# Kernel optimization log

Hardware: AMD Instinct MI355X
Metric: run time of the kernel (lower is better)

The kernel has to match this reference:

```python
import jax, jax.numpy as jnp
import numpy as np

N_NODES = 100000
N_EDGES = 1000000
D_IN = 64
D_OUT = 64


def setup_inputs() -> dict:
    key = jax.random.key(0)
    k_x, k_e, k_wl, k_bl, k_wr = jax.random.split(key, 5)
    x = jax.random.normal(k_x, (N_NODES, D_IN), dtype=jnp.float32)
    edge_index = jax.random.randint(k_e, (2, N_EDGES), 0, N_NODES, dtype=jnp.int64)
    scale = 1.0 / np.sqrt(D_IN)
    # SAGEConv params: lin_l (neighbor path, with bias), lin_r (root/self path, no bias)
    W_l = jax.random.uniform(k_wl, (D_OUT, D_IN), dtype=jnp.float32, minval=-scale, maxval=scale)
    b_l = jax.random.uniform(k_bl, (D_OUT,), dtype=jnp.float32, minval=-scale, maxval=scale)
    W_r = jax.random.uniform(k_wr, (D_OUT, D_IN), dtype=jnp.float32, minval=-scale, maxval=scale)
    return {"x": x, "edge_index": edge_index, "W_l": W_l, "b_l": b_l, "W_r": W_r}


def reference(x, edge_index, W_l, b_l, W_r):
    # PyG SAGEConv with mean aggregation:
    #   out = lin_l(mean_{j in N(i)} x_j) + lin_r(x_i);  then ReLU (from GCN.forward)
    src = edge_index[0]  # message sources
    dst = edge_index[1]  # aggregation targets
    n = x.shape[0]
    msg = x[src]  # [E, D_IN] gather
    agg = jax.ops.segment_sum(msg, dst, num_segments=n)  # [N, D_IN]
    deg = jax.ops.segment_sum(jnp.ones((src.shape[0],), x.dtype), dst, num_segments=n)
    mean = agg / jnp.maximum(deg, 1.0)[:, None]  # isolated nodes -> 0
    out = mean @ W_l.T + b_l + x @ W_r.T
    return jax.nn.relu(out)
```

## Files before the change

kernel.cpp:

```cpp
#include <hip/hip_runtime.h>

#define N_NODES 100000
#define N_EDGES 1000000
#define D 64

#define NFINE 782
#define CAP2 1536
#define CHUNK 4096
#define EDGE_BLOCKS 245
#define CONV_BLOCKS 6250
#define CONS_BLOCKS 782
#define STR 132

typedef unsigned short u16;
typedef unsigned int u32;
using bf16x8 = __attribute__((ext_vector_type(8))) short;
using f32x4  = __attribute__((ext_vector_type(4))) float;

__device__ __forceinline__ u16 f2bf(float f) {
    u32 u = __float_as_uint(f);
    return (u16)((u + 0x7FFF + ((u >> 16) & 1)) >> 16);
}
__device__ __forceinline__ float bf2f(u16 v) {
    return __uint_as_float(((u32)v) << 16);
}

__global__ __launch_bounds__(256) void conv_zero_kernel(
    const float* __restrict__ x, u16* __restrict__ xb,
    int* __restrict__ cur2) {
    if (blockIdx.x == CONV_BLOCKS) {
        for (int j = threadIdx.x; j < NFINE; j += 256) cur2[j] = 0;
        return;
    }
    int i = blockIdx.x * 256 + threadIdx.x;
    float4 v = ((const float4*)x)[i];
    ((ushort4*)xb)[i] = make_ushort4(f2bf(v.x), f2bf(v.y), f2bf(v.z), f2bf(v.w));
}

__global__ __launch_bounds__(1024) void build3_kernel(
    const int* __restrict__ ei, int* __restrict__ cur2,
    u32* __restrict__ pairs2) {
    __shared__ u32 sorted[CHUNK];
    __shared__ u16 binof[CHUNK];
    __shared__ int hist[NFINE];
    __shared__ int off_l[NFINE];
    __shared__ int cur_l[NFINE];
    __shared__ int base_g[NFINE];
    __shared__ int wsum[16];

    int b = blockIdx.x;
    int t = threadIdx.x;
    int ln = t & 63;
    int wv = t >> 6;

    const u32* uu = (const u32*)ei;
    int f = 1;
    #pragma unroll
    for (int i = 1; i < 16; i += 2)
        if (uu[i] != 0u) f = 0;

    if (t < NFINE) hist[t] = 0;
    __syncthreads();

    int e0 = b * CHUNK;
    int e1 = min(e0 + CHUNK, N_EDGES);
    int ne = e1 - e0;

    int srcv[4], dstv[4];
    #pragma unroll
    for (int i = 0; i < 4; i++) {
        int ee = e0 + t + i * 1024;
        bool ok = ee < e1;
        srcv[i] = ok ? (f ? ei[2 * ee] : ei[ee]) : 0;
        dstv[i] = ok ? (f ? ei[2 * (N_EDGES + ee)] : ei[N_EDGES + ee]) : -1;
    }
    #pragma unroll
    for (int i = 0; i < 4; i++)
        if (dstv[i] >= 0) atomicAdd(&hist[dstv[i] >> 7], 1);
    __syncthreads();

    int h = (t < NFINE) ? hist[t] : 0;
    int inc = h;
    #pragma unroll
    for (int o = 1; o < 64; o <<= 1) {
        int v = __shfl_up(inc, o);
        if (ln >= o) inc += v;
    }
    if (ln == 63) wsum[wv] = inc;
    __syncthreads();
    if (t < 16) {
        int w = wsum[t];
        int winc = w;
        #pragma unroll
        for (int o = 1; o < 16; o <<= 1) {
            int v = __shfl_up(winc, o);
            if (t >= o) winc += v;
        }
        wsum[t] = winc - w;
    }
    __syncthreads();
    if (t < NFINE) {
        int ex = inc - h + wsum[wv];
        off_l[t] = ex;
        cur_l[t] = ex;
        base_g[t] = h ? atomicAdd(&cur2[t], h) : 0;
    }
    __syncthreads();

    #pragma unroll
    for (int i = 0; i < 4; i++) {
        if (dstv[i] >= 0) {
            int fine = dstv[i] >> 7;
            int slot = atomicAdd(&cur_l[fine], 1);
            sorted[slot] = (u32)srcv[i] | ((u32)(dstv[i] & 127) << 17);
            binof[slot] = (u16)fine;
        }
    }
    __syncthreads();

    for (int i = t; i < ne; i += 1024) {
        int fine = binof[i];
        int pos = base_g[fine] + (i - off_l[fine]);
        if (pos < CAP2)
            pairs2[(size_t)fine * CAP2 + pos] = sorted[i];
    }
}

__global__ __launch_bounds__(1024, 8) void cons3_kernel(
    const u16* __restrict__ xb, const float* __restrict__ Wl,
    const float* __restrict__ bl, const float* __restrict__ Wr,
    const int* __restrict__ cur2, const u32* __restrict__ pairs2,
    float* __restrict__ out) {
    __shared__ u16 Bs[64 * STR];
    __shared__ u16 As[128 * STR];
    __shared__ int sorted_s[CAP2];
    __shared__ int deg_l[128];
    __shared__ int off_l[128];
    __shared__ int cur_l[128];

    int tid = threadIdx.x;
    int bin = blockIdx.x;
    int nbase = bin * 128;
    int lane = tid & 63;
    int wv = tid >> 6;

    if (tid < 128) { deg_l[tid] = 0; cur_l[tid] = 0; }
    for (int i = tid; i < CAP2; i += 1024) sorted_s[i] = 0;

    if (tid < 256) {
        int row = tid >> 2;
        int seg = tid & 3;
        const float4* wlf = (const float4*)Wl;
        const float4* wrf = (const float4*)Wr;
        #pragma unroll
        for (int j = 0; j < 4; j++) {
            float4 a = wlf[row * 16 + seg * 4 + j];
            float4 bq = wrf[row * 16 + seg * 4 + j];
            *(ushort4*)&Bs[row * STR + seg * 16 + j * 4] =
                make_ushort4(f2bf(a.x), f2bf(a.y), f2bf(a.z), f2bf(a.w));
            *(ushort4*)&Bs[row * STR + 64 + seg * 16 + j * 4] =
                make_ushort4(f2bf(bq.x), f2bf(bq.y), f2bf(bq.z), f2bf(bq.w));
        }
    }

    int cnt = min(cur2[bin], CAP2);
    const u32* pb = &pairs2[(size_t)bin * CAP2];
    u32 ve[2];
    #pragma unroll
    for (int i = 0; i < 2; i++) {
        int e = tid + i * 1024;
        ve[i] = (e < cnt) ? pb[e] : 0xFFFFFFFFu;
    }
    __syncthreads();

    #pragma unroll
    for (int i = 0; i < 2; i++)
        if (ve[i] != 0xFFFFFFFFu) atomicAdd(&deg_l[ve[i] >> 17], 1);
    __syncthreads();

    if (tid < 64) {
        int d0 = deg_l[2 * tid], d1 = deg_l[2 * tid + 1];
        int s = d0 + d1;
        int inc = s;
        #pragma unroll
        for (int o = 1; o < 64; o <<= 1) {
            int v = __shfl_up(inc, o);
            if (tid >= o) inc += v;
        }
        int ex = inc - s;
        off_l[2 * tid] = ex;
        off_l[2 * tid + 1] = ex + d0;
    }
    __syncthreads();

    #pragma unroll
    for (int i = 0; i < 2; i++) {
        u32 v = ve[i];
        if (v != 0xFFFFFFFFu) {
            int dl = (int)(v >> 17);
            int p = off_l[dl] + atomicAdd(&cur_l[dl], 1);
            sorted_s[p] = (int)(v & 0x1FFFFu);
        }
    }
    __syncthreads();

    int nl8 = lane >> 3;
    int c = lane & 7;
    int nl = wv * 8 + nl8;
    int n = nbase + nl;
    int d = deg_l[nl];
    int st = off_l[nl];

    int maxd = d;
    maxd = max(maxd, __shfl_xor(maxd, 8));
    maxd = max(maxd, __shfl_xor(maxd, 16));
    maxd = max(maxd, __shfl_xor(maxd, 32));

    float acc[8];
    #pragma unroll
    for (int j = 0; j < 8; j++) acc[j] = 0.0f;

    for (int k = 0; k < maxd; k += 2) {
        int i0 = max(st + min(k, d - 1), 0);
        int i1 = max(st + min(k + 1, d - 1), 0);
        int s0 = sorted_s[i0];
        int s1 = sorted_s[i1];
        float m0 = (k < d) ? 1.0f : 0.0f;
        float m1 = (k + 1 < d) ? 1.0f : 0.0f;
        bf16x8 r0 = *(const bf16x8*)&xb[(size_t)s0 * D + c * 8];
        bf16x8 r1 = *(const bf16x8*)&xb[(size_t)s1 * D + c * 8];
        #pragma unroll
        for (int j = 0; j < 8; j++)
            acc[j] = fmaf(m0, bf2f((u16)r0[j]), acc[j]);
        #pragma unroll
        for (int j = 0; j < 8; j++)
            acc[j] = fmaf(m1, bf2f((u16)r1[j]), acc[j]);
    }

    float inv = (d > 0) ? (1.0f / (float)d) : 0.0f;
    bf16x8 p;
    #pragma unroll
    for (int j = 0; j < 8; j++) p[j] = (short)f2bf(acc[j] * inv);
    *(bf16x8*)&As[nl * STR + c * 8] = p;
    bf16x8 xr = {0, 0, 0, 0, 0, 0, 0, 0};
    if (n < N_NODES) xr = *(const bf16x8*)&xb[(size_t)n * D + c * 8];
    *(bf16x8*)&As[nl * STR + 64 + c * 8] = xr;
    __syncthreads();

    int mtile = wv >> 1;
    int nt0 = (wv & 1) * 2;
    int lrow = lane & 15;
    int quad = lane >> 4;

    const u16* Ab  = &As[(mtile * 16 + lrow) * STR + quad * 8];
    const u16* Bb0 = &Bs[((nt0 + 0) * 16 + lrow) * STR + quad * 8];
    const u16* Bb1 = &Bs[((nt0 + 1) * 16 + lrow) * STR + quad * 8];

    float bias0 = bl[(nt0 + 0) * 16 + lrow];
    float bias1 = bl[(nt0 + 1) * 16 + lrow];
    f32x4 acc0 = {bias0, bias0, bias0, bias0};
    f32x4 acc1 = {bias1, bias1, bias1, bias1};

    #pragma unroll
    for (int kk = 0; kk < 4; kk++) {
        bf16x8 af = *(const bf16x8*)&Ab[kk * 32];
        bf16x8 b0 = *(const bf16x8*)&Bb0[kk * 32];
        bf16x8 b1 = *(const bf16x8*)&Bb1[kk * 32];
        acc0 = __builtin_amdgcn_mfma_f32_16x16x32_bf16(af, b0, acc0, 0, 0, 0);
        acc1 = __builtin_amdgcn_mfma_f32_16x16x32_bf16(af, b1, acc1, 0, 0, 0);
    }

    int node = nbase + mtile * 16 + quad * 4;
    #pragma unroll
    for (int r = 0; r < 4; r++) {
        if (node + r < N_NODES) {
            out[(size_t)(node + r) * D + (nt0 + 0) * 16 + lrow] = fmaxf(acc0[r], 0.0f);
            out[(size_t)(node + r) * D + (nt0 + 1) * 16 + lrow] = fmaxf(acc1[r], 0.0f);
        }
    }
}

extern "C" void kernel_launch(void* const* d_in, const int* in_sizes, int n_in,
                              void* d_out, int out_size, void* d_ws, size_t ws_size,
                              hipStream_t stream) {
    const float* x  = (const float*)d_in[0];
    const int*   ei = (const int*)d_in[1];
    const float* Wl = (const float*)d_in[2];
    const float* bl = (const float*)d_in[3];
    const float* Wr = (const float*)d_in[4];
    float* out = (float*)d_out;

    char* p = (char*)d_ws;
    int* cur2   = (int*)p;                        p += 1024 * sizeof(int);
    u32* pairs2 = (u32*)p;                        p += (size_t)NFINE * CAP2 * sizeof(u32);
    u16* xb     = (u16*)p;

    conv_zero_kernel<<<CONV_BLOCKS + 1, 256, 0, stream>>>(x, xb, cur2);
    build3_kernel<<<EDGE_BLOCKS, 1024, 0, stream>>>(ei, cur2, pairs2);
    cons3_kernel<<<CONS_BLOCKS, 1024, 0, stream>>>(xb, Wl, bl, Wr, cur2, pairs2, out);
}
```

Measured before the change: 143.0 us.

## Split consumer blocks into two 64-node halves and unroll gather by four

The consumer kernel now launches two 512-thread blocks per 128-node bin. Each block keeps only the edges of its 64-node half, which shrinks shared memory and raises the number of blocks that can be resident. The gather loop is unrolled to four neighbor rows per iteration to put more loads in flight. The edge-index reads for int64 inputs now use single 8-byte loads. The cost is that both halves re-read the whole bin's pair list and repeat the weight conversion. The tail of the matmul section is not shown, so whether it was adapted to 64 rows and 512 threads is unclear.

After: 137.6 us. 1.04x faster.

```diff
diff --git a/kernel.cpp b/kernel.cpp
--- a/kernel.cpp
+++ b/kernel.cpp
@@ -9,8 +9,9 @@
 #define CHUNK 4096
 #define EDGE_BLOCKS 245
 #define CONV_BLOCKS 6250
-#define CONS_BLOCKS 782
+#define CONS_BLOCKS 1564
 #define STR 132
+#define SCAP 1024
 
 typedef unsigned short u16;
 typedef unsigned int u32;
@@ -66,13 +67,21 @@
     int e1 = min(e0 + CHUNK, N_EDGES);
     int ne = e1 - e0;
 
+    const uint2* e64 = (const uint2*)ei;
     int srcv[4], dstv[4];
     #pragma unroll
     for (int i = 0; i < 4; i++) {
         int ee = e0 + t + i * 1024;
         bool ok = ee < e1;
-        srcv[i] = ok ? (f ? ei[2 * ee] : ei[ee]) : 0;
-        dstv[i] = ok ? (f ? ei[2 * (N_EDGES + ee)] : ei[N_EDGES + ee]) : -1;
+        if (f) {
+            uint2 sv = ok ? e64[ee] : make_uint2(0u, 0u);
+            uint2 dv = ok ? e64[N_EDGES + ee] : make_uint2(0u, 0u);
+            srcv[i] = (int)sv.x;
+            dstv[i] = ok ? (int)dv.x : -1;
+        } else {
+            srcv[i] = ok ? ei[ee] : 0;
+            dstv[i] = ok ? ei[N_EDGES + ee] : -1;
+        }
     }
     #pragma unroll
     for (int i = 0; i < 4; i++)
@@ -126,26 +135,38 @@
     }
 }
 
-__global__ __launch_bounds__(1024, 8) void cons3_kernel(
+__global__ __launch_bounds__(512, 8) void cons4_kernel(
     const u16* __restrict__ xb, const float* __restrict__ Wl,
     const float* __restrict__ bl, const float* __restrict__ Wr,
     const int* __restrict__ cur2, const u32* __restrict__ pairs2,
     float* __restrict__ out) {
     __shared__ u16 Bs[64 * STR];
-    __shared__ u16 As[128 * STR];
-    __shared__ int sorted_s[CAP2];
-    __shared__ int deg_l[128];
-    __shared__ int off_l[128];
-    __shared__ int cur_l[128];
+    __shared__ u16 As[64 * STR];
+    __shared__ int sorted_s[SCAP];
+    __shared__ int deg_l[64];
+    __shared__ int off_l[64];
+    __shared__ int cur_l[64];
 
     int tid = threadIdx.x;
-    int bin = blockIdx.x;
-    int nbase = bin * 128;
+    int bin = blockIdx.x >> 1;
+    int half = blockIdx.x & 1;
+    int nbase = bin * 128 + half * 64;
+    if (nbase >= N_NODES) return;
+
     int lane = tid & 63;
     int wv = tid >> 6;
 
-    if (tid < 128) { deg_l[tid] = 0; cur_l[tid] = 0; }
-    for (int i = tid; i < CAP2; i += 1024) sorted_s[i] = 0;
+    int cnt = min(cur2[bin], CAP2);
+    const u32* pb = &pairs2[(size_t)bin * CAP2];
+    u32 ve[3];
+    #pragma unroll
+    for (int i = 0; i < 3; i++) {
+        int e = tid + i * 512;
+        ve[i] = (e < cnt) ? pb[e] : 0xFFFFFFFFu;
+    }
+
+    if (tid < 64) { deg_l[tid] = 0; cur_l[tid] = 0; }
+    if (tid == 0) sorted_s[0] = 0;
 
     if (tid < 256) {
         int row = tid >> 2;
@@ -162,44 +183,34 @@
                 make_ushort4(f2bf(bq.x), f2bf(bq.y), f2bf(bq.z), f2bf(bq.w));
         }
     }
-
-    int cnt = min(cur2[bin], CAP2);
-    const u32* pb = &pairs2[(size_t)bin * CAP2];
-    u32 ve[2];
-    #pragma unroll
-    for (int i = 0; i < 2; i++) {
-        int e = tid + i * 1024;
-        ve[i] = (e < cnt) ? pb[e] : 0xFFFFFFFFu;
-    }
-    __syncthreads();
-
-    #pragma unroll
-    for (int i = 0; i < 2; i++)
-        if (ve[i] != 0xFFFFFFFFu) atomicAdd(&deg_l[ve[i] >> 17], 1);
+    __syncthreads();
+
+    #pragma unroll
+    for (int i = 0; i < 3; i++) {
+        u32 v = ve[i];
+        if ((int)(v >> 23) == half) atomicAdd(&deg_l[(v >> 17) & 63], 1);
+    }
     __syncthreads();
 
     if (tid < 64) {
-        int d0 = deg_l[2 * tid], d1 = deg_l[2 * tid + 1];
-        int s = d0 + d1;
-        int inc = s;
+        int dd = deg_l[tid];
+        int inc = dd;
         #pragma unroll
         for (int o = 1; o < 64; o <<= 1) {
             int v = __shfl_up(inc, o);
-            if (tid >= o) inc += v;
-        }
-        int ex = inc - s;
-        off_l[2 * tid] = ex;
-        off_l[2 * tid + 1] = ex + d0;
-    }
-    __syncthreads();
-
-    #pragma unroll
-    for (int i = 0; i < 2; i++) {
+            if (lane >= o) inc += v;
+        }
+        off_l[tid] = inc - dd;
+    }
+    __syncthreads();
+
+    #pragma unroll
+    for (int i = 0; i < 3; i++) {
         u32 v = ve[i];
-        if (v != 0xFFFFFFFFu) {
-            int dl = (int)(v >> 17);
-            int p = off_l[dl] + atomicAdd(&cur_l[dl], 1);
-            sorted_s[p] = (int)(v & 0x1FFFFu);
+        if ((int)(v >> 23) == half) {
+            int ln = (v >> 17) & 63;
+            int p = off_l[ln] + atomicAdd(&cur_l[ln], 1);
+            if (p < SCAP) sorted_s[p] = (int)(v & 0x1FFFFu);
         }
     }
     __syncthreads();
@@ -220,21 +231,37 @@
     #pragma unroll
     for (int j = 0; j < 8; j++) acc[j] = 0.0f;
 
-    for (int k = 0; k < maxd; k += 2) {
-        int i0 = max(st + min(k, d - 1), 0);
-        int i1 = max(st + min(k + 1, d - 1), 0);
+    int dm1 = (d > 0) ? (d - 1) : 0;
+    int sb = (d > 0) ? st : 0;
+    for (int k = 0; k < maxd; k += 4) {
+        int i0 = sb + min(k + 0, dm1);
+        int i1 = sb + min(k + 1, dm1);
+        int i2 = sb + min(k + 2, dm1);
+        int i3 = sb + min(k + 3, dm1);
         int s0 = sorted_s[i0];
         int s1 = sorted_s[i1];
-        float m0 = (k < d) ? 1.0f : 0.0f;
-        float m1 = (k + 1 < d) ? 1.0f : 0.0f;
+        int s2 = sorted_s[i2];
+        int s3 = sorted_s[i3];
         bf16x8 r0 = *(const bf16x8*)&xb[(size_t)s0 * D + c * 8];
         bf16x8 r1 = *(const bf16x8*)&xb[(size_t)s1 * D + c * 8];
+        bf16x8 r2 = *(const bf16x8*)&xb[(size_t)s2 * D + c * 8];
+        bf16x8 r3 = *(const bf16x8*)&xb[(size_t)s3 * D + c * 8];
+        float m0 = (k + 0 < d) ? 1.0f : 0.0f;
+        float m1 = (k + 1 < d) ? 1.0f : 0.0f;
+        float m2 = (k + 2 < d) ? 1.0f : 0.0f;
+        float m3 = (k + 3 < d) ? 1.0f : 0.0f;
         #pragma unroll
         for (int j = 0; j < 8; j++)
             acc[j] = fmaf(m0, bf2f((u16)r0[j]), acc[j]);
         #pragma unroll
         for (int j = 0; j < 8; j++)
             acc[j] = fmaf(m1, bf2f((u16)r1[j]), acc[j]);
+        #pragma unroll
+        for (int j = 0; j < 8; j++)
+            acc[j] = fmaf(m2, bf2f((u16)r2[j]), acc[j]);
+        #pragma unroll
+        for (int j = 0; j < 8; j++)
+            acc[j] = fmaf(m3, bf2f((u16)r3[j]), acc[j]);
     }
 
     float inv = (d > 0) ? (1.0f / (float)d) : 0.0f;
@@ -297,5 +324,5 @@
 
     conv_zero_kernel<<<CONV_BLOCKS + 1, 256, 0, stream>>>(x, xb, cur2);
     build3_kernel<<<EDGE_BLOCKS, 1024, 0, stream>>>(ei, cur2, pairs2);
-    cons3_kernel<<<CONS_BLOCKS, 1024, 0, stream>>>(xb, Wl, bl, Wr, cur2, pairs2, out);
-}
+    cons4_kernel<<<CONS_BLOCKS, 512, 0, stream>>>(xb, Wl, bl, Wr, cur2, pairs2, out);
+}
```
